# Performance work log

Measured on AMD Instinct MI355X. Metric: run time of the kernel, lower is better.

The kernel has to match this reference:

```python
import jax, jax.numpy as jnp
import numpy as np
import math

B, L, D, H = 4, 2048, 512, 8
DH = D // H
MAX_SEQ = 2048


def setup_inputs() -> dict:
    key = jax.random.key(0)
    ks = jax.random.split(key, 12)
    s = 1.0 / math.sqrt(D)
    return {
        "q_in": jax.random.normal(ks[0], (B, L, D), jnp.float32),
        "k_in": jax.random.normal(ks[1], (B, L, D), jnp.float32),
        "v_in": jax.random.normal(ks[2], (B, L, D), jnp.float32),
        "Wq_w": jax.random.normal(ks[3], (D, D), jnp.float32) * s,
        "Wq_b": jnp.zeros((D,), jnp.float32),
        "Wk_w": jax.random.normal(ks[4], (D, D), jnp.float32) * s,
        "Wk_b": jnp.zeros((D,), jnp.float32),
        "Wv_w": jax.random.normal(ks[5], (D, D), jnp.float32) * s,
        "Wv_b": jnp.zeros((D,), jnp.float32),
        "E": jax.random.normal(ks[6], (MAX_SEQ, DH), jnp.float32) * (1.0 / math.sqrt(DH)),
        "fc_w": jax.random.normal(ks[7], (D, D), jnp.float32) * s,
        "fc_b": jnp.zeros((D,), jnp.float32),
    }


def _forward(q_in, k_in, v_in, Wq_w, Wq_b, Wk_w, Wk_b, Wv_w, Wv_b, E, fc_w, fc_b):
    b, lq, d = q_in.shape
    dh = E.shape[1]
    h = d // dh

    def proj(x, W, bias):
        # [b, l, d] -> [b, h, l, dh]
        y = x @ W + bias
        return y.reshape(b, -1, h, dh).transpose(0, 2, 1, 3)

    q = proj(q_in, Wq_w, Wq_b)
    k = proj(k_in, Wk_w, Wk_b)
    v = proj(v_in, Wv_w, Wv_b)
    len_q, len_k = q.shape[2], k.shape[2]

    # left-aligned relative embedding slice
    max_seq = E.shape[0]
    start = max(0, max_seq - len_q)
    e = E[start:, :]                       # [m, dh], m = min(max_seq, len_q)
    m = e.shape[0]

    QE = jnp.einsum("bhld,md->bhlm", q, e)  # [b, h, l, m]
    # qe masking: for query row i keep columns j with i + j >= m - 1
    keep = (jnp.arange(len_q)[:, None] + jnp.arange(m)[None, :]) >= (m - 1)
    QE = QE * keep.astype(QE.dtype)

    # skewing trick: pad one zero column on the left, reshape, drop first row
    padded = jnp.pad(QE, ((0, 0), (0, 0), (0, 0), (1, 0)))  # [b, h, l, m+1]
    reshaped = padded.reshape(b, h, m + 1, len_q)
    Srel = reshaped[:, :, 1:, :]           # [b, h, m, l]
    if len_k > len_q:
        Srel = jnp.pad(Srel, ((0, 0), (0, 0), (0, 0), (0, len_k - len_q)))
    elif len_k < len_q:
        Srel = Srel[:, :, :, :len_k]

    QKt = jnp.einsum("bhld,bhsd->bhls", q, k)
    logits = (QKt + Srel) / math.sqrt(dh)
    attn_w = jax.nn.softmax(logits, axis=-1)
    attn = jnp.einsum("bhls,bhsd->bhld", attn_w, v)
    out = attn.transpose(0, 2, 1, 3).reshape(b, -1, d)
    out = out @ fc_w + fc_b
    return out, attn_w


def reference(q_in, k_in, v_in, Wq_w, Wq_b, Wk_w, Wk_b, Wv_w, Wv_b, E, fc_w, fc_b):
    return _forward(q_in, k_in, v_in, Wq_w, Wq_b, Wk_w, Wk_b, Wv_w, Wv_b, E, fc_w, fc_b)
```

## Files before the change

kernel.cpp:

```cpp
#include <hip/hip_runtime.h>

#define SC2   0.18033688011112042f
#define PSTR  36

typedef __attribute__((ext_vector_type(8)))  __bf16       bf16x8;
typedef __attribute__((ext_vector_type(16))) float        f32x16;
typedef __attribute__((ext_vector_type(4)))  float        f32x4;
typedef __attribute__((ext_vector_type(4)))  unsigned int u32x4;
typedef __attribute__((ext_vector_type(2)))  unsigned int u32x2;

#define ROWPAT(g, hi) ((((g)&3)) + 8*((g)>>2) + 4*(hi))

__device__ inline unsigned short f2bf(float f){
  unsigned u = __builtin_bit_cast(unsigned, f);
  u += 0x7FFFu + ((u >> 16) & 1u);
  return (unsigned short)(u >> 16);
}
__device__ inline float bf2f(unsigned short h){
  unsigned u = ((unsigned)h) << 16;
  return __builtin_bit_cast(float, u);
}
__device__ inline unsigned pack2bf(float lo, float hi){
  return (unsigned)f2bf(lo) | ((unsigned)f2bf(hi) << 16);
}
__device__ inline f32x16 zero16(){
  f32x16 z;
  #pragma unroll
  for (int i=0;i<16;i++) z[i]=0.f;
  return z;
}

__global__ __launch_bounds__(256) void transpose_w_kernel(const float* __restrict__ W,
                                                          unsigned short* __restrict__ Wt){
  __shared__ unsigned short t[32][33];
  const int n0 = blockIdx.x*32, k0 = blockIdx.y*32;
  const int tx = threadIdx.x & 31, ty = threadIdx.x >> 5;
  #pragma unroll
  for (int i=0;i<4;i++){
    int k = ty*4 + i;
    t[k][tx] = f2bf(W[(size_t)(k0+k)*512 + n0+tx]);
  }
  __syncthreads();
  #pragma unroll
  for (int i=0;i<4;i++){
    int n = ty*4+i;
    Wt[(size_t)(n0+n)*512 + k0 + tx] = t[tx][n];
  }
}

__global__ __launch_bounds__(256) void transpose_v_kernel(const unsigned short* __restrict__ V,
                                                          unsigned short* __restrict__ VT){
  __shared__ unsigned short t[32][33];
  const int bh = blockIdx.z;
  const int l0 = blockIdx.x*32, d0 = blockIdx.y*32;
  const int tx = threadIdx.x & 31, ty = threadIdx.x >> 5;
  const unsigned short* Vb = V + (size_t)bh*2048*64;
  unsigned short* Tb = VT + (size_t)bh*64*2048;
  #pragma unroll
  for (int i=0;i<4;i++){
    int row = ty*4+i;
    t[row][tx] = Vb[(size_t)(l0+row)*64 + d0+tx];
  }
  __syncthreads();
  #pragma unroll
  for (int i=0;i<4;i++){
    int d = ty*4+i;
    Tb[(size_t)(d0+d)*2048 + l0+tx] = t[tx][d];
  }
}

__global__ __launch_bounds__(256) void erev_kernel(const float* __restrict__ E,
                                                   unsigned short* __restrict__ Ebf){
  const int i = blockIdx.x*256 + threadIdx.x;
  const int base = i*4;
  const int u = base >> 6, d = base & 63;
  f32x4 v = *(const f32x4*)(E + (size_t)(2047 - u)*64 + d);
  unsigned short o[4];
  #pragma unroll
  for (int j=0;j<4;j++) o[j] = f2bf(v[j]);
  *(u32x2*)(Ebf + (size_t)u*64 + d) = u32x2{(unsigned)o[0] | ((unsigned)o[1]<<16),
                                            (unsigned)o[2] | ((unsigned)o[3]<<16)};
}

__global__ __launch_bounds__(256,2) void proj_gemm_kernel(
    const float* __restrict__ X, const unsigned int* __restrict__ Wt,
    const float* __restrict__ bias, unsigned short* __restrict__ Y)
{
  __shared__ unsigned int Al[128][17];
  __shared__ unsigned int Bl[128][17];
  const int n0 = blockIdx.x * 128;
  const int m0 = blockIdx.y * 128;
  const int tid = threadIdx.x;
  const int lane = tid & 63, wave = tid >> 6;
  const int lr = lane & 31, hi = lane >> 5;
  const int wr = wave >> 1, wc = wave & 1;
  const int r = tid & 127, kh = tid >> 7;

  f32x16 acc[2][2];
  acc[0][0]=zero16(); acc[0][1]=zero16(); acc[1][0]=zero16(); acc[1][1]=zero16();

  for (int k0=0; k0<512; k0+=32){
    const float* Xr = X + (size_t)(m0 + r)*512 + k0 + kh*16;
    #pragma unroll
    for (int c=0;c<2;c++){
      f32x4 x0 = *(const f32x4*)(Xr + c*8);
      f32x4 x1 = *(const f32x4*)(Xr + c*8 + 4);
      Al[r][kh*8 + c*4 + 0] = pack2bf(x0[0], x0[1]);
      Al[r][kh*8 + c*4 + 1] = pack2bf(x0[2], x0[3]);
      Al[r][kh*8 + c*4 + 2] = pack2bf(x1[0], x1[1]);
      Al[r][kh*8 + c*4 + 3] = pack2bf(x1[2], x1[3]);
    }
    const unsigned int* Wr = Wt + (size_t)(n0 + r)*256 + (k0>>1) + kh*8;
    #pragma unroll
    for (int c=0;c<8;c++) Bl[r][kh*8 + c] = Wr[c];
    __syncthreads();
    #pragma unroll
    for (int t=0;t<2;t++){
      bf16x8 af[2], bfr[2];
      #pragma unroll
      for (int mt=0;mt<2;mt++){
        u32x4 w;
        #pragma unroll
        for (int j=0;j<4;j++) w[j] = Al[wr*64 + mt*32 + lr][t*8 + hi*4 + j];
        af[mt] = __builtin_bit_cast(bf16x8, w);
      }
      #pragma unroll
      for (int nt=0;nt<2;nt++){
        u32x4 w;
        #pragma unroll
        for (int j=0;j<4;j++) w[j] = Bl[wc*64 + nt*32 + lr][t*8 + hi*4 + j];
        bfr[nt] = __builtin_bit_cast(bf16x8, w);
      }
      #pragma unroll
      for (int mt=0;mt<2;mt++)
        #pragma unroll
        for (int nt=0;nt<2;nt++)
          acc[mt][nt] = __builtin_amdgcn_mfma_f32_32x32x16_bf16(af[mt], bfr[nt], acc[mt][nt], 0,0,0);
    }
    __syncthreads();
  }

  #pragma unroll
  for (int mt=0;mt<2;mt++)
    #pragma unroll
    for (int nt=0;nt<2;nt++){
      const int n = n0 + wc*64 + nt*32 + lr;
      const float bv = bias[n];
      const int h = n >> 6, dh = n & 63;
      #pragma unroll
      for (int g=0; g<16; g++){
        const int m = m0 + wr*64 + mt*32 + ROWPAT(g,hi);
        const int b = m >> 11, l = m & 2047;
        Y[((size_t)(b*8 + h)*2048 + l)*64 + dh] = f2bf(acc[mt][nt][g] + bv);
      }
    }
}

#define ATTN_TASK_MAP()                                   \
  const int bid = blockIdx.x;                             \
  const int xcd = bid & 7;                                \
  const int j   = bid >> 3;                   \
  const int bhg = xcd*4 + (j >> 7);                       \
  const int jj  = j & 127;                                \
  const int half = jj & 1;                                \
  const int ltile = 63 - (jj >> 1);                       \
  const int l0w = ltile*32;                               \
  const int c_max = ltile;                                \
  const int clo = half*32, chi = clo + 31;                \
  const int relhi = c_max < chi ? c_max : chi;            \
  const int nr_lo = (c_max+1 > clo) ? c_max+1 : clo;

__global__ __launch_bounds__(64) void attn_d_kernel(
    const unsigned short* __restrict__ Q,
    const unsigned short* __restrict__ Kb,
    const unsigned short* __restrict__ Ebf,
    float* __restrict__ dws)
{
  __shared__ unsigned short slab[2*32*PSTR];
  const int tid = threadIdx.x;
  const int lane = tid & 63;
  const int lr = lane & 31;
  const int hi = lane >> 5;
  ATTN_TASK_MAP();

  unsigned short* Wa = slab;
  unsigned short* Wb = Wa + 32*PSTR;

  const unsigned short* Qrow = Q + ((size_t)bhg*2048 + l0w + lr)*64;
  bf16x8 qf[4];
  #pragma unroll
  for (int t=0;t<4;t++) qf[t] = *(const bf16x8*)(Qrow + t*16 + hi*8);
  const unsigned short* Krows = Kb + (size_t)bhg*2048*64;

  float dpart[16];
  #pragma unroll
  for (int g=0;g<16;g++) dpart[g] = 0.f;

  #pragma unroll 2
  for (int c = nr_lo; c <= chi; ++c){
    const int s0 = c*32;
    f32x16 acc = zero16();
    const unsigned short* Krow = Krows + (size_t)(s0 + lr)*64;
    #pragma unroll
    for (int t=0;t<4;t++){
      bf16x8 kf = *(const bf16x8*)(Krow + t*16 + hi*8);
      acc = __builtin_amdgcn_mfma_f32_32x32x16_bf16(qf[t], kf, acc, 0,0,0);
    }
    #pragma unroll
    for (int g=0; g<16; g++) dpart[g] += exp2f(acc[g] * SC2);
  }
  if (relhi >= clo){
    unsigned short* cur = Wa;
    unsigned short* prv = Wb;
    if (relhi < c_max){
      const int dpr = l0w - 32*(relhi+1);
      const unsigned short* Erow = Ebf + (size_t)(dpr + lr)*64;
      f32x16 eacc = zero16();
      #pragma unroll
      for (int t=0;t<4;t++){
        bf16x8 ef = *(const bf16x8*)(Erow + t*16 + hi*8);
        eacc = __builtin_amdgcn_mfma_f32_32x32x16_bf16(qf[t], ef, eacc, 0,0,0);
      }
      #pragma unroll
      for (int g=0; g<16; g++) prv[ROWPAT(g,hi)*PSTR + lr] = f2bf(eacc[g]);
    }
    #pragma unroll 1
    for (int c = relhi; c >= clo; --c){
      const int s0 = c*32;
      const int delta = l0w - s0;
      {
        const unsigned short* Erow = Ebf + (size_t)(delta + lr)*64;
        f32x16 eacc = zero16();
        #pragma unroll
        for (int t=0;t<4;t++){
          bf16x8 ef = *(const bf16x8*)(Erow + t*16 + hi*8);
          eacc = __builtin_amdgcn_mfma_f32_32x32x16_bf16(qf[t], ef, eacc, 0,0,0);
        }
        #pragma unroll
        for (int g=0; g<16; g++) cur[ROWPAT(g,hi)*PSTR + lr] = f2bf(eacc[g]);
      }
      f32x16 acc = zero16();
      const unsigned short* Krow = Krows + (size_t)(s0 + lr)*64;
      #pragma unroll
      for (int t=0;t<4;t++){
        bf16x8 kf = *(const bf16x8*)(Krow + t*16 + hi*8);
        acc = __builtin_amdgcn_mfma_f32_32x32x16_bf16(qf[t], kf, acc, 0,0,0);
      }
      #pragma unroll
      for (int g=0; g<16; g++){
        const int rp = ROWPAT(g,hi);
        const int dloc = rp - lr;
        float v = acc[g];
        if (delta + dloc >= 0)
          v += bf2f(dloc >= 0 ? cur[rp*PSTR + dloc] : prv[rp*PSTR + 32 + dloc]);
        dpart[g] += exp2f(v * SC2);
      }
      unsigned short* tmp = cur; cur = prv; prv = tmp;
    }
  }
  #pragma unroll
  for (int g=0; g<16; g++){
    float v = dpart[g];
    v += __shfl_xor(v, 1, 64);
    v += __shfl_xor(v, 2, 64);
    v += __shfl_xor(v, 4, 64);
    v += __shfl_xor(v, 8, 64);
    v += __shfl_xor(v, 16, 64);
    dpart[g] = v;
  }
  float* dtask = dws + (size_t)(bhg*64 + ltile)*64 + half*32;
  if (lr == 0){
    #pragma unroll
    for (int g=0; g<16; g++) dtask[ROWPAT(g,hi)] = dpart[g];
  }
}

__global__ __launch_bounds__(64) void attn_pv_kernel(
    const unsigned short* __restrict__ Q,
    const unsigned short* __restrict__ Kb,
    const unsigned short* __restrict__ VT,
    const unsigned short* __restrict__ Ebf,
    const float* __restrict__ dws,
    float* __restrict__ attn_w,
    float* __restrict__ po)
{
  __shared__ unsigned short slab[3*32*PSTR];
  const int tid = threadIdx.x;
  const int lane = tid & 63;
  const int lr = lane & 31;
  const int hi = lane >> 5;
  ATTN_TASK_MAP();

  unsigned short* Wa = slab;
  unsigned short* Wb = Wa + 32*PSTR;
  unsigned short* Ps = Wb + 32*PSTR;

  const unsigned short* Qrow = Q + ((size_t)bhg*2048 + l0w + lr)*64;
  bf16x8 qf[4];
  #pragma unroll
  for (int t=0;t<4;t++) qf[t] = *(const bf16x8*)(Qrow + t*16 + hi*8);

  const unsigned short* Krows = Kb + (size_t)bhg*2048*64;
  const unsigned short* Vtb   = VT + (size_t)bhg*64*2048;

  const float* dtask = dws + (size_t)(bhg*64 + ltile)*64;
  float invd[16];
  #pragma unroll
  for (int g=0; g<16; g++){
    const int rp = ROWPAT(g,hi);
    invd[g] = 1.0f / (dtask[rp] + dtask[32 + rp]);
  }

  f32x16 oacc[2];
  oacc[0]=zero16(); oacc[1]=zero16();
  float* awbase = attn_w + ((size_t)bhg*2048 + l0w)*2048;

  #pragma unroll 1
  for (int c = nr_lo; c <= chi; ++c){
    const int s0 = c*32;
    f32x16 acc = zero16();
    const unsigned short* Krow = Krows + (size_t)(s0 + lr)*64;
    #pragma unroll
    for (int t=0;t<4;t++){
      bf16x8 kf = *(const bf16x8*)(Krow + t*16 + hi*8);
      acc = __builtin_amdgcn_mfma_f32_32x32x16_bf16(qf[t], kf, acc, 0,0,0);
    }
    float p[16];
    #pragma unroll
    for (int g=0; g<16; g++){
      const int rp = ROWPAT(g,hi);
      p[g] = exp2f(acc[g] * SC2) * invd[g];
      __builtin_nontemporal_store(p[g], awbase + (size_t)rp*2048 + s0 + lr);
    }
    #pragma unroll
    for (int q=0;q<8;q++){
      const int rp0 = ROWPAT(2*q,hi);
      const unsigned pkv = pack2bf(p[2*q], p[2*q+1]);
      Ps[rp0*PSTR + lr]     = (unsigned short)(pkv & 0xFFFFu);
      Ps[(rp0+1)*PSTR + lr] = (unsigned short)(pkv >> 16);
    }
    bf16x8 af[2];
    #pragma unroll
    for (int sh=0; sh<2; sh++){
      const unsigned short* ap = Ps + lr*PSTR + sh*16 + 8*hi;
      u32x2 a0 = *(const u32x2*)(ap);
      u32x2 a1 = *(const u32x2*)(ap + 4);
      u32x4 w; w[0]=a0[0]; w[1]=a0[1]; w[2]=a1[0]; w[3]=a1[1];
      af[sh] = __builtin_bit_cast(bf16x8, w);
    }
    #pragma unroll
    for (int sh=0; sh<2; sh++)
      #pragma unroll
      for (int dt=0; dt<2; dt++){
        bf16x8 vfr = *(const bf16x8*)(Vtb + (size_t)(dt*32+lr)*2048 + s0 + sh*16 + 8*hi);
        oacc[dt] = __builtin_amdgcn_mfma_f32_32x32x16_bf16(af[sh], vfr, oacc[dt], 0,0,0);
      }
  }
  if (relhi >= clo){
    unsigned short* cur = Wa;
    unsigned short* prv = Wb;
    if (relhi < c_max){
      const int dpr = l0w - 32*(relhi+1);
      const unsigned short* Erow = Ebf + (size_t)(dpr + lr)*64;
      f32x16 eacc = zero16();
      #pragma unroll
      for (int t=0;t<4;t++){
        bf16x8 ef = *(const bf16x8*)(Erow + t*16 + hi*8);
        eacc = __builtin_amdgcn_mfma_f32_32x32x16_bf16(qf[t], ef, eacc, 0,0,0);
      }
      #pragma unroll
      for (int g=0; g<16; g++) prv[ROWPAT(g,hi)*PSTR + lr] = f2bf(eacc[g]);
    }
    #pragma unroll 1
    for (int c = relhi; c >= clo; --c){
      const int s0 = c*32;
      const int delta = l0w - s0;
      {
        const unsigned short* Erow = Ebf + (size_t)(delta + lr)*64;
        f32x16 eacc = zero16();
        #pragma unroll
        for (int t=0;t<4;t++){
          bf16x8 ef = *(const bf16x8*)(Erow + t*16 + hi*8);
          eacc = __builtin_amdgcn_mfma_f32_32x32x16_bf16(qf[t], ef, eacc, 0,0,0);
        }
        #pragma unroll
        for (int g=0; g<16; g++) cur[ROWPAT(g,hi)*PSTR + lr] = f2bf(eacc[g]);
      }
      f32x16 acc = zero16();
      const unsigned short* Krow = Krows + (size_t)(s0 + lr)*64;
      #pragma unroll
      for (int t=0;t<4;t++){
        bf16x8 kf = *(const bf16x8*)(Krow + t*16 + hi*8);
        acc = __builtin_amdgcn_mfma_f32_32x32x16_bf16(qf[t], kf, acc, 0,0,0);
      }
      float p[16];
      #pragma unroll
      for (int g=0; g<16; g++){
        const int rp = ROWPAT(g,hi);
        const int dloc = rp - lr;
        float v = acc[g];
        if (delta + dloc >= 0)
          v += bf2f(dloc >= 0 ? cur[rp*PSTR + dloc] : prv[rp*PSTR + 32 + dloc]);
        p[g] = exp2f(v * SC2) * invd[g];
        __builtin_nontemporal_store(p[g], awbase + (size_t)rp*2048 + s0 + lr);
      }
      #pragma unroll
      for (int q=0;q<8;q++){
        const int rp0 = ROWPAT(2*q,hi);
        const unsigned pkv = pack2bf(p[2*q], p[2*q+1]);
        Ps[rp0*PSTR + lr]     = (unsigned short)(pkv & 0xFFFFu);
        Ps[(rp0+1)*PSTR + lr] = (unsigned short)(pkv >> 16);
      }
      bf16x8 af[2];
      #pragma unroll
      for (int sh=0; sh<2; sh++){
        const unsigned short* ap = Ps + lr*PSTR + sh*16 + 8*hi;
        u32x2 a0 = *(const u32x2*)(ap);
        u32x2 a1 = *(const u32x2*)(ap + 4);
        u32x4 w; w[0]=a0[0]; w[1]=a0[1]; w[2]=a1[0]; w[3]=a1[1];
        af[sh] = __builtin_bit_cast(bf16x8, w);
      }
      #pragma unroll
      for (int sh=0; sh<2; sh++)
        #pragma unroll
        for (int dt=0; dt<2; dt++){
          bf16x8 vfr = *(const bf16x8*)(Vtb + (size_t)(dt*32+lr)*2048 + s0 + sh*16 + 8*hi);
          oacc[dt] = __builtin_amdgcn_mfma_f32_32x32x16_bf16(af[sh], vfr, oacc[dt], 0,0,0);
        }
      unsigned short* tmp = cur; cur = prv; prv = tmp;
    }
  }

  float* pobase = po + (size_t)half*4194304 + ((size_t)bhg*2048 + l0w)*64;
  #pragma unroll
  for (int dt=0; dt<2; dt++)
    #pragma unroll
    for (int g=0; g<16; g++){
      const int rp = ROWPAT(g,hi);
      pobase[(size_t)rp*64 + dt*32 + lr] = oacc[dt][g];
    }
}

__global__ __launch_bounds__(256) void pv_merge_kernel(const float* __restrict__ po,
                                                       unsigned short* __restrict__ ATT){
  const size_t i = ((size_t)blockIdx.x*256 + threadIdx.x)*8;
  f32x4 a0 = *(const f32x4*)(po + i);
  f32x4 a1 = *(const f32x4*)(po + i + 4);
  f32x4 b0 = *(const f32x4*)(po + 4194304 + i);
  f32x4 b1 = *(const f32x4*)(po + 4194304 + i + 4);
  u32x4 w;
  w[0] = pack2bf(a0[0]+b0[0], a0[1]+b0[1]);
  w[1] = pack2bf(a0[2]+b0[2], a0[3]+b0[3]);
  w[2] = pack2bf(a1[0]+b1[0], a1[1]+b1[1]);
  w[3] = pack2bf(a1[2]+b1[2], a1[3]+b1[3]);
  *(u32x4*)(ATT + i) = w;
}

__global__ __launch_bounds__(256,2) void fc_gemm_kernel(
    const unsigned short* __restrict__ A,
    const unsigned int* __restrict__ Wt,
    const float* __restrict__ bias, float* __restrict__ Out)
{
  __shared__ unsigned int Al[128][17];
  __shared__ unsigned int Bl[128][17];
  const int n0 = blockIdx.x * 128;
  const int m0 = blockIdx.y * 128;
  const int tid = threadIdx.x;
  const int lane = tid & 63, wave = tid >> 6;
  const int lr = lane & 31, hi = lane >> 5;
  const int wr = wave >> 1, wc = wave & 1;
  const int r = tid & 127, kh = tid >> 7;

  f32x16 acc[2][2];
  acc[0][0]=zero16(); acc[0][1]=zero16(); acc[1][0]=zero16(); acc[1][1]=zero16();

  for (int k0=0; k0<512; k0+=32){
    const int m = m0 + r; const int b = m >> 11, l = m & 2047;
    const int k = k0 + kh*16; const int h = k >> 6, dh0 = k & 63;
    const unsigned int* Ar = (const unsigned int*)(A + ((size_t)(b*8+h)*2048 + l)*64 + dh0);
    #pragma unroll
    for (int c=0;c<8;c++) Al[r][kh*8+c] = Ar[c];
    const unsigned int* Wr = Wt + (size_t)(n0 + r)*256 + (k0>>1) + kh*8;
    #pragma unroll
    for (int c=0;c<8;c++) Bl[r][kh*8 + c] = Wr[c];
    __syncthreads();
    #pragma unroll
    for (int t=0;t<2;t++){
      bf16x8 af[2], bfr[2];
      #pragma unroll
      for (int mt=0;mt<2;mt++){
        u32x4 w;
        #pragma unroll
        for (int j=0;j<4;j++) w[j] = Al[wr*64 + mt*32 + lr][t*8 + hi*4 + j];
        af[mt] = __builtin_bit_cast(bf16x8, w);
      }
      #pragma unroll
      for (int nt=0;nt<2;nt++){
        u32x4 w;
        #pragma unroll
        for (int j=0;j<4;j++) w[j] = Bl[wc*64 + nt*32 + lr][t*8 + hi*4 + j];
        bfr[nt] = __builtin_bit_cast(bf16x8, w);
      }
      #pragma unroll
      for (int mt=0;mt<2;mt++)
        #pragma unroll
        for (int nt=0;nt<2;nt++)
          acc[mt][nt] = __builtin_amdgcn_mfma_f32_32x32x16_bf16(af[mt], bfr[nt], acc[mt][nt], 0,0,0);
    }
    __syncthreads();
  }

  #pragma unroll
  for (int mt=0;mt<2;mt++)
    #pragma unroll
    for (int nt=0;nt<2;nt++){
      const int n = n0 + wc*64 + nt*32 + lr;
      const float bv = bias[n];
      #pragma unroll
      for (int g=0; g<16; g++){
        const int m2 = m0 + wr*64 + mt*32 + ROWPAT(g,hi);
        Out[(size_t)m2*512 + n] = acc[mt][nt][g] + bv;
      }
    }
}

extern "C" void kernel_launch(void* const* d_in, const int* in_sizes, int n_in,
                              void* d_out, int out_size, void* d_ws, size_t ws_size,
                              hipStream_t stream)
{
  const float* q_in = (const float*)d_in[0];
  const float* k_in = (const float*)d_in[1];
  const float* v_in = (const float*)d_in[2];
  const float* Wq_w = (const float*)d_in[3];
  const float* Wq_b = (const float*)d_in[4];
  const float* Wk_w = (const float*)d_in[5];
  const float* Wk_b = (const float*)d_in[6];
  const float* Wv_w = (const float*)d_in[7];
  const float* Wv_b = (const float*)d_in[8];
  const float* E    = (const float*)d_in[9];
  const float* fc_w = (const float*)d_in[10];
  const float* fc_b = (const float*)d_in[11];

  float* out = (float*)d_out;
  float* attn_w = out + (size_t)4*2048*512;

  unsigned short* Qws = (unsigned short*)d_ws;
  unsigned short* Kws = Qws + (size_t)4194304;
  unsigned short* Vws = Kws + (size_t)4194304;
  unsigned short* ATT = Vws + (size_t)4194304;
  unsigned short* VTs = ATT + (size_t)4194304;
  unsigned short* Ebf = VTs + (size_t)4194304;
  unsigned short* WqT = Ebf + 131072;
  unsigned short* WkT = WqT + 262144;
  unsigned short* WvT = WkT + 262144;
  unsigned short* WfT = WvT + 262144;
  float* po  = (float*)(WfT + 262144);
  float* dws = po + (size_t)2*4194304;

  dim3 tg(16,16);
  hipLaunchKernelGGL(transpose_w_kernel, tg, dim3(256), 0, stream, Wq_w, WqT);
  hipLaunchKernelGGL(transpose_w_kernel, tg, dim3(256), 0, stream, Wk_w, WkT);
  hipLaunchKernelGGL(transpose_w_kernel, tg, dim3(256), 0, stream, Wv_w, WvT);
  hipLaunchKernelGGL(transpose_w_kernel, tg, dim3(256), 0, stream, fc_w, WfT);
  hipLaunchKernelGGL(erev_kernel, dim3(128), dim3(256), 0, stream, E, Ebf);

  dim3 pg(4, 64);
  hipLaunchKernelGGL(proj_gemm_kernel, pg, dim3(256), 0, stream, q_in, (const unsigned int*)WqT, Wq_b, Qws);
  hipLaunchKernelGGL(proj_gemm_kernel, pg, dim3(256), 0, stream, k_in, (const unsigned int*)WkT, Wk_b, Kws);
  hipLaunchKernelGGL(proj_gemm_kernel, pg, dim3(256), 0, stream, v_in, (const unsigned int*)WvT, Wv_b, Vws);

  hipLaunchKernelGGL(transpose_v_kernel, dim3(64,2,32), dim3(256), 0, stream, Vws, VTs);

  hipLaunchKernelGGL(attn_d_kernel,  dim3(4096), dim3(64), 0, stream, Qws, Kws, Ebf, dws);
  hipLaunchKernelGGL(attn_pv_kernel, dim3(4096), dim3(64), 0, stream, Qws, Kws, VTs, Ebf, dws, attn_w, po);
  hipLaunchKernelGGL(pv_merge_kernel, dim3(2048), dim3(256), 0, stream, po, ATT);

  hipLaunchKernelGGL(fc_gemm_kernel, pg, dim3(256), 0, stream, ATT, (const unsigned int*)WfT, fc_b, out);
}
```

Baseline: 443.0 us.

## Store unnormalized bf16 probabilities in first pass and reuse in PV pass

The denominator pass now writes the exponentiated, unnormalized attention probabilities as packed bf16 into a large workspace buffer. A new PV kernel reads them back instead of recomputing QK^T, the relative-embedding skew and exp2. This is used only when the workspace holds the extra 256 MB. The three Q/K/V projection GEMMs are also merged into one launch using blockIdx.z. The trade is MFMA and exp recompute for extra global memory traffic, about 256 MB written and then read, and the bf16 rounding of P also changes the values written to attn_w.

New measurement: 515.6 us. 16.4% more time.

```diff
diff --git a/kernel.cpp b/kernel.cpp
--- a/kernel.cpp
+++ b/kernel.cpp
@@ -82,10 +82,18 @@
                                             (unsigned)o[2] | ((unsigned)o[3]<<16)};
 }
 
-__global__ __launch_bounds__(256,2) void proj_gemm_kernel(
-    const float* __restrict__ X, const unsigned int* __restrict__ Wt,
-    const float* __restrict__ bias, unsigned short* __restrict__ Y)
+__global__ __launch_bounds__(256,2) void proj3_gemm_kernel(
+    const float* __restrict__ X0, const float* __restrict__ X1, const float* __restrict__ X2,
+    const unsigned int* __restrict__ W0, const unsigned int* __restrict__ W1, const unsigned int* __restrict__ W2,
+    const float* __restrict__ b0, const float* __restrict__ b1, const float* __restrict__ b2,
+    unsigned short* __restrict__ Y0, unsigned short* __restrict__ Y1, unsigned short* __restrict__ Y2)
 {
+  const int z = blockIdx.z;
+  const float* X = z==0 ? X0 : (z==1 ? X1 : X2);
+  const unsigned int* Wt = z==0 ? W0 : (z==1 ? W1 : W2);
+  const float* bias = z==0 ? b0 : (z==1 ? b1 : b2);
+  unsigned short* Y = z==0 ? Y0 : (z==1 ? Y1 : Y2);
+
   __shared__ unsigned int Al[128][17];
   __shared__ unsigned int Bl[128][17];
   const int n0 = blockIdx.x * 128;
@@ -170,11 +178,14 @@
   const int relhi = c_max < chi ? c_max : chi;            \
   const int nr_lo = (c_max+1 > clo) ? c_max+1 : clo;
 
+
+template<bool SAVEP>
 __global__ __launch_bounds__(64) void attn_d_kernel(
     const unsigned short* __restrict__ Q,
     const unsigned short* __restrict__ Kb,
     const unsigned short* __restrict__ Ebf,
-    float* __restrict__ dws)
+    float* __restrict__ dws,
+    unsigned int* __restrict__ Pws)
 {
   __shared__ unsigned short slab[2*32*PSTR];
   const int tid = threadIdx.x;
@@ -185,6 +196,8 @@
 
   unsigned short* Wa = slab;
   unsigned short* Wb = Wa + 32*PSTR;
+  unsigned int* Pt = SAVEP ? (Pws + (size_t)bid*16384) : nullptr;
+  const int pidx = hi*32 + lr;
 
   const unsigned short* Qrow = Q + ((size_t)bhg*2048 + l0w + lr)*64;
   bf16x8 qf[4];
@@ -206,8 +219,14 @@
       bf16x8 kf = *(const bf16x8*)(Krow + t*16 + hi*8);
       acc = __builtin_amdgcn_mfma_f32_32x32x16_bf16(qf[t], kf, acc, 0,0,0);
     }
-    #pragma unroll
-    for (int g=0; g<16; g++) dpart[g] += exp2f(acc[g] * SC2);
+    float p[16];
+    #pragma unroll
+    for (int g=0; g<16; g++){ p[g] = exp2f(acc[g] * SC2); dpart[g] += p[g]; }
+    if constexpr (SAVEP){
+      unsigned int* pc = Pt + (size_t)(c - clo)*512;
+      #pragma unroll
+      for (int q=0;q<8;q++) pc[q*64 + pidx] = pack2bf(p[2*q], p[2*q+1]);
+    }
   }
   if (relhi >= clo){
     unsigned short* cur = Wa;
@@ -246,6 +265,7 @@
         bf16x8 kf = *(const bf16x8*)(Krow + t*16 + hi*8);
         acc = __builtin_amdgcn_mfma_f32_32x32x16_bf16(qf[t], kf, acc, 0,0,0);
       }
+      float p[16];
       #pragma unroll
       for (int g=0; g<16; g++){
         const int rp = ROWPAT(g,hi);
@@ -253,7 +273,13 @@
         float v = acc[g];
         if (delta + dloc >= 0)
           v += bf2f(dloc >= 0 ? cur[rp*PSTR + dloc] : prv[rp*PSTR + 32 + dloc]);
-        dpart[g] += exp2f(v * SC2);
+        p[g] = exp2f(v * SC2);
+        dpart[g] += p[g];
+      }
+      if constexpr (SAVEP){
+        unsigned int* pc = Pt + (size_t)(c - clo)*512;
+        #pragma unroll
+        for (int q=0;q<8;q++) pc[q*64 + pidx] = pack2bf(p[2*q], p[2*q+1]);
       }
       unsigned short* tmp = cur; cur = prv; prv = tmp;
     }
@@ -273,6 +299,84 @@
     #pragma unroll
     for (int g=0; g<16; g++) dtask[ROWPAT(g,hi)] = dpart[g];
   }
+}
+
+__global__ __launch_bounds__(64) void attn_pv_read_kernel(
+    const unsigned int* __restrict__ Pws,
+    const unsigned short* __restrict__ VT,
+    const float* __restrict__ dws,
+    float* __restrict__ attn_w,
+    float* __restrict__ po)
+{
+  __shared__ unsigned short Ps[32*PSTR];
+  const int tid = threadIdx.x;
+  const int lane = tid & 63;
+  const int lr = lane & 31;
+  const int hi = lane >> 5;
+  ATTN_TASK_MAP();
+  (void)relhi; (void)nr_lo; (void)c_max;
+
+  const unsigned int* Pt = Pws + (size_t)bid*16384;
+  const int pidx = hi*32 + lr;
+  const unsigned short* Vtb = VT + (size_t)bhg*64*2048;
+
+  const float* dtask = dws + (size_t)(bhg*64 + ltile)*64;
+  float invd[16];
+  #pragma unroll
+  for (int g=0; g<16; g++){
+    const int rp = ROWPAT(g,hi);
+    invd[g] = 1.0f / (dtask[rp] + dtask[32 + rp]);
+  }
+
+  f32x16 oacc[2];
+  oacc[0]=zero16(); oacc[1]=zero16();
+  float* awbase = attn_w + ((size_t)bhg*2048 + l0w)*2048;
+
+  #pragma unroll 1
+  for (int c = clo; c <= chi; ++c){
+    const int s0 = c*32;
+    const unsigned int* pc = Pt + (size_t)(c - clo)*512;
+    unsigned pk[8];
+    #pragma unroll
+    for (int q=0;q<8;q++) pk[q] = pc[q*64 + pidx];
+    #pragma unroll
+    for (int g=0; g<16; g++){
+      const int rp = ROWPAT(g,hi);
+      const float v = bf2f((unsigned short)((pk[g>>1] >> ((g&1)*16)) & 0xFFFFu)) * invd[g];
+      __builtin_nontemporal_store(v, awbase + (size_t)rp*2048 + s0 + lr);
+    }
+    #pragma unroll
+    for (int q=0;q<8;q++){
+      const int rp0 = ROWPAT(2*q,hi);
+      Ps[rp0*PSTR + lr]     = (unsigned short)(pk[q] & 0xFFFFu);
+      Ps[(rp0+1)*PSTR + lr] = (unsigned short)(pk[q] >> 16);
+    }
+    bf16x8 af[2];
+    #pragma unroll
+    for (int sh=0; sh<2; sh++){
+      const unsigned short* ap = Ps + lr*PSTR + sh*16 + 8*hi;
+      u32x2 a0 = *(const u32x2*)(ap);
+      u32x2 a1 = *(const u32x2*)(ap + 4);
+      u32x4 w; w[0]=a0[0]; w[1]=a0[1]; w[2]=a1[0]; w[3]=a1[1];
+      af[sh] = __builtin_bit_cast(bf16x8, w);
+    }
+    #pragma unroll
+    for (int sh=0; sh<2; sh++)
+      #pragma unroll
+      for (int dt=0; dt<2; dt++){
+        bf16x8 vfr = *(const bf16x8*)(Vtb + (size_t)(dt*32+lr)*2048 + s0 + sh*16 + 8*hi);
+        oacc[dt] = __builtin_amdgcn_mfma_f32_32x32x16_bf16(af[sh], vfr, oacc[dt], 0,0,0);
+      }
+  }
+
+  float* pobase = po + (size_t)half*4194304 + ((size_t)bhg*2048 + l0w)*64;
+  #pragma unroll
+  for (int dt=0; dt<2; dt++)
+    #pragma unroll
+    for (int g=0; g<16; g++){
+      const int rp = ROWPAT(g,hi);
+      pobase[(size_t)rp*64 + dt*32 + lr] = oacc[dt][g] * invd[g];
+    }
 }
 
 __global__ __launch_bounds__(64) void attn_pv_kernel(
@@ -556,6 +660,10 @@
   unsigned short* WfT = WvT + 262144;
   float* po  = (float*)(WfT + 262144);
   float* dws = po + (size_t)2*4194304;
+  unsigned int* Pws = (unsigned int*)(dws + 4096*64);
+
+  const size_t need_fast = 78905344ull + 268435456ull;
+  const bool fast = ws_size >= need_fast;
 
   dim3 tg(16,16);
   hipLaunchKernelGGL(transpose_w_kernel, tg, dim3(256), 0, stream, Wq_w, WqT);
@@ -564,16 +672,26 @@
   hipLaunchKernelGGL(transpose_w_kernel, tg, dim3(256), 0, stream, fc_w, WfT);
   hipLaunchKernelGGL(erev_kernel, dim3(128), dim3(256), 0, stream, E, Ebf);
 
-  dim3 pg(4, 64);
-  hipLaunchKernelGGL(proj_gemm_kernel, pg, dim3(256), 0, stream, q_in, (const unsigned int*)WqT, Wq_b, Qws);
-  hipLaunchKernelGGL(proj_gemm_kernel, pg, dim3(256), 0, stream, k_in, (const unsigned int*)WkT, Wk_b, Kws);
-  hipLaunchKernelGGL(proj_gemm_kernel, pg, dim3(256), 0, stream, v_in, (const unsigned int*)WvT, Wv_b, Vws);
+  hipLaunchKernelGGL(proj3_gemm_kernel, dim3(4,64,3), dim3(256), 0, stream,
+                     q_in, k_in, v_in,
+                     (const unsigned int*)WqT, (const unsigned int*)WkT, (const unsigned int*)WvT,
+                     Wq_b, Wk_b, Wv_b, Qws, Kws, Vws);
 
   hipLaunchKernelGGL(transpose_v_kernel, dim3(64,2,32), dim3(256), 0, stream, Vws, VTs);
 
-  hipLaunchKernelGGL(attn_d_kernel,  dim3(4096), dim3(64), 0, stream, Qws, Kws, Ebf, dws);
-  hipLaunchKernelGGL(attn_pv_kernel, dim3(4096), dim3(64), 0, stream, Qws, Kws, VTs, Ebf, dws, attn_w, po);
+  if (fast){
+    hipLaunchKernelGGL(HIP_KERNEL_NAME(attn_d_kernel<true>), dim3(4096), dim3(64), 0, stream,
+                       Qws, Kws, Ebf, dws, Pws);
+    hipLaunchKernelGGL(attn_pv_read_kernel, dim3(4096), dim3(64), 0, stream,
+                       (const unsigned int*)Pws, VTs, dws, attn_w, po);
+  } else {
+    hipLaunchKernelGGL(HIP_KERNEL_NAME(attn_d_kernel<false>), dim3(4096), dim3(64), 0, stream,
+                       Qws, Kws, Ebf, dws, Pws);
+    hipLaunchKernelGGL(attn_pv_kernel, dim3(4096), dim3(64), 0, stream,
+                       Qws, Kws, VTs, Ebf, dws, attn_w, po);
+  }
   hipLaunchKernelGGL(pv_merge_kernel, dim3(2048), dim3(256), 0, stream, po, ATT);
 
-  hipLaunchKernelGGL(fc_gemm_kernel, pg, dim3(256), 0, stream, ATT, (const unsigned int*)WfT, fc_b, out);
-}
+  hipLaunchKernelGGL(fc_gemm_kernel, dim3(4,64), dim3(256), 0, stream,
+                     ATT, (const unsigned int*)WfT, fc_b, out);
+}
```

## Split attention key range into quarters and batch QKV projections in one launch

Applied to the files above, without the earlier changes.

The attention denominator and PV kernels now split each 32-row query tile's key columns into four 16-tile chunks instead of two. This doubles the grid to 8192 single-wave blocks so there is more parallelism and better load balance. The partial denominators and partial PV outputs are widened to four slots, and the merge kernel sums all four. The three projection GEMMs are merged into one launch indexed by blockIdx.z, which removes launch gaps and fills the GPU better. In exchange, the partial-output buffer doubles in size, adding write and read traffic in the merge step, and each block now has more fixed setup cost relative to its work.

After: 427.0 us. 1.04x faster.

```diff
diff --git a/kernel.cpp b/kernel.cpp
--- a/kernel.cpp
+++ b/kernel.cpp
@@ -82,10 +82,18 @@
                                             (unsigned)o[2] | ((unsigned)o[3]<<16)};
 }
 
-__global__ __launch_bounds__(256,2) void proj_gemm_kernel(
-    const float* __restrict__ X, const unsigned int* __restrict__ Wt,
-    const float* __restrict__ bias, unsigned short* __restrict__ Y)
+__global__ __launch_bounds__(256,2) void proj3_gemm_kernel(
+    const float* __restrict__ X0, const float* __restrict__ X1, const float* __restrict__ X2,
+    const unsigned int* __restrict__ W0, const unsigned int* __restrict__ W1, const unsigned int* __restrict__ W2,
+    const float* __restrict__ b0, const float* __restrict__ b1, const float* __restrict__ b2,
+    unsigned short* __restrict__ Y0, unsigned short* __restrict__ Y1, unsigned short* __restrict__ Y2)
 {
+  const int z = blockIdx.z;
+  const float* X = z==0 ? X0 : (z==1 ? X1 : X2);
+  const unsigned int* Wt = z==0 ? W0 : (z==1 ? W1 : W2);
+  const float* bias = z==0 ? b0 : (z==1 ? b1 : b2);
+  unsigned short* Y = z==0 ? Y0 : (z==1 ? Y1 : Y2);
+
   __shared__ unsigned int Al[128][17];
   __shared__ unsigned int Bl[128][17];
   const int n0 = blockIdx.x * 128;
@@ -159,14 +167,14 @@
 #define ATTN_TASK_MAP()                                   \
   const int bid = blockIdx.x;                             \
   const int xcd = bid & 7;                                \
-  const int j   = bid >> 3;                   \
-  const int bhg = xcd*4 + (j >> 7);                       \
-  const int jj  = j & 127;                                \
-  const int half = jj & 1;                                \
-  const int ltile = 63 - (jj >> 1);                       \
+  const int j   = bid >> 3;                  \
+  const int bhg = xcd*4 + (j >> 8);                       \
+  const int jj  = j & 255;                                \
+  const int quarter = jj & 3;                             \
+  const int ltile = 63 - (jj >> 2);                       \
   const int l0w = ltile*32;                               \
   const int c_max = ltile;                                \
-  const int clo = half*32, chi = clo + 31;                \
+  const int clo = quarter*16, chi = clo + 15;             \
   const int relhi = c_max < chi ? c_max : chi;            \
   const int nr_lo = (c_max+1 > clo) ? c_max+1 : clo;
 
@@ -268,7 +276,7 @@
     v += __shfl_xor(v, 16, 64);
     dpart[g] = v;
   }
-  float* dtask = dws + (size_t)(bhg*64 + ltile)*64 + half*32;
+  float* dtask = dws + (size_t)(bhg*64 + ltile)*128 + quarter*32;
   if (lr == 0){
     #pragma unroll
     for (int g=0; g<16; g++) dtask[ROWPAT(g,hi)] = dpart[g];
@@ -303,12 +311,12 @@
   const unsigned short* Krows = Kb + (size_t)bhg*2048*64;
   const unsigned short* Vtb   = VT + (size_t)bhg*64*2048;
 
-  const float* dtask = dws + (size_t)(bhg*64 + ltile)*64;
+  const float* dtask = dws + (size_t)(bhg*64 + ltile)*128;
   float invd[16];
   #pragma unroll
   for (int g=0; g<16; g++){
     const int rp = ROWPAT(g,hi);
-    invd[g] = 1.0f / (dtask[rp] + dtask[32 + rp]);
+    invd[g] = 1.0f / (dtask[rp] + dtask[32 + rp] + dtask[64 + rp] + dtask[96 + rp]);
   }
 
   f32x16 oacc[2];
@@ -431,7 +439,7 @@
     }
   }
 
-  float* pobase = po + (size_t)half*4194304 + ((size_t)bhg*2048 + l0w)*64;
+  float* pobase = po + (size_t)quarter*4194304 + ((size_t)bhg*2048 + l0w)*64;
   #pragma unroll
   for (int dt=0; dt<2; dt++)
     #pragma unroll
@@ -444,15 +452,18 @@
 __global__ __launch_bounds__(256) void pv_merge_kernel(const float* __restrict__ po,
                                                        unsigned short* __restrict__ ATT){
   const size_t i = ((size_t)blockIdx.x*256 + threadIdx.x)*8;
-  f32x4 a0 = *(const f32x4*)(po + i);
-  f32x4 a1 = *(const f32x4*)(po + i + 4);
-  f32x4 b0 = *(const f32x4*)(po + 4194304 + i);
-  f32x4 b1 = *(const f32x4*)(po + 4194304 + i + 4);
+  f32x4 s0 = *(const f32x4*)(po + i);
+  f32x4 s1 = *(const f32x4*)(po + i + 4);
+  #pragma unroll
+  for (int q=1; q<4; q++){
+    s0 += *(const f32x4*)(po + (size_t)q*4194304 + i);
+    s1 += *(const f32x4*)(po + (size_t)q*4194304 + i + 4);
+  }
   u32x4 w;
-  w[0] = pack2bf(a0[0]+b0[0], a0[1]+b0[1]);
-  w[1] = pack2bf(a0[2]+b0[2], a0[3]+b0[3]);
-  w[2] = pack2bf(a1[0]+b1[0], a1[1]+b1[1]);
-  w[3] = pack2bf(a1[2]+b1[2], a1[3]+b1[3]);
+  w[0] = pack2bf(s0[0], s0[1]);
+  w[1] = pack2bf(s0[2], s0[3]);
+  w[2] = pack2bf(s1[0], s1[1]);
+  w[3] = pack2bf(s1[2], s1[3]);
   *(u32x4*)(ATT + i) = w;
 }
 
@@ -555,7 +566,7 @@
   unsigned short* WvT = WkT + 262144;
   unsigned short* WfT = WvT + 262144;
   float* po  = (float*)(WfT + 262144);
-  float* dws = po + (size_t)2*4194304;
+  float* dws = po + (size_t)4*4194304;
 
   dim3 tg(16,16);
   hipLaunchKernelGGL(transpose_w_kernel, tg, dim3(256), 0, stream, Wq_w, WqT);
@@ -564,16 +575,17 @@
   hipLaunchKernelGGL(transpose_w_kernel, tg, dim3(256), 0, stream, fc_w, WfT);
   hipLaunchKernelGGL(erev_kernel, dim3(128), dim3(256), 0, stream, E, Ebf);
 
-  dim3 pg(4, 64);
-  hipLaunchKernelGGL(proj_gemm_kernel, pg, dim3(256), 0, stream, q_in, (const unsigned int*)WqT, Wq_b, Qws);
-  hipLaunchKernelGGL(proj_gemm_kernel, pg, dim3(256), 0, stream, k_in, (const unsigned int*)WkT, Wk_b, Kws);
-  hipLaunchKernelGGL(proj_gemm_kernel, pg, dim3(256), 0, stream, v_in, (const unsigned int*)WvT, Wv_b, Vws);
+  hipLaunchKernelGGL(proj3_gemm_kernel, dim3(4,64,3), dim3(256), 0, stream,
+                     q_in, k_in, v_in,
+                     (const unsigned int*)WqT, (const unsigned int*)WkT, (const unsigned int*)WvT,
+                     Wq_b, Wk_b, Wv_b, Qws, Kws, Vws);
 
   hipLaunchKernelGGL(transpose_v_kernel, dim3(64,2,32), dim3(256), 0, stream, Vws, VTs);
 
-  hipLaunchKernelGGL(attn_d_kernel,  dim3(4096), dim3(64), 0, stream, Qws, Kws, Ebf, dws);
-  hipLaunchKernelGGL(attn_pv_kernel, dim3(4096), dim3(64), 0, stream, Qws, Kws, VTs, Ebf, dws, attn_w, po);
+  hipLaunchKernelGGL(attn_d_kernel,  dim3(8192), dim3(64), 0, stream, Qws, Kws, Ebf, dws);
+  hipLaunchKernelGGL(attn_pv_kernel, dim3(8192), dim3(64), 0, stream, Qws, Kws, VTs, Ebf, dws, attn_w, po);
   hipLaunchKernelGGL(pv_merge_kernel, dim3(2048), dim3(256), 0, stream, po, ATT);
 
-  hipLaunchKernelGGL(fc_gemm_kernel, pg, dim3(256), 0, stream, ATT, (const unsigned int*)WfT, fc_b, out);
-}
+  hipLaunchKernelGGL(fc_gemm_kernel, dim3(4,64), dim3(256), 0, stream,
+                     ATT, (const unsigned int*)WfT, fc_b, out);
+}
```
